# Optimization experiments

Measured on AMD Instinct MI355X. Metric: run time of the kernel, lower is better.

## Reference

```python
import jax, jax.numpy as jnp
import numpy as np

BITS = 4
PACK = 32 // BITS            # 8 nibbles per int32
IN, OUT = 4096, 4096
NNZ = 75008


def setup_inputs() -> dict:
    key = jax.random.key(0)
    ks = jax.random.split(key, 7)
    x = jax.random.normal(ks[0], (4, 2048, IN), jnp.float32)
    # packed 4-bit indices: any int32 bit pattern is valid after masking
    qweight = jax.random.randint(ks[1], (IN // PACK, OUT), 0, 2147483647, jnp.int32)
    lookup_table = jax.random.normal(ks[2], (OUT, 2 ** BITS), jnp.float32)
    bias = jax.random.normal(ks[3], (OUT,), jnp.float32)
    rows = jnp.sort(jax.random.randint(ks[4], (OUT + 1,), 0, NNZ, jnp.int32))
    outlier_rows = rows.at[0].set(0).at[-1].set(NNZ)  # valid CSR crow
    outlier_cols = jax.random.randint(ks[5], (NNZ,), 0, IN, jnp.int32)
    outlier_vals = jax.random.normal(ks[6], (NNZ,), jnp.float32)
    return {
        'x': x,
        'lookup_table': lookup_table,
        'bias': bias,
        'outlier_vals': outlier_vals,
        'qweight': qweight,
        'outlier_rows': outlier_rows,
        'outlier_cols': outlier_cols,
    }


def _dequant_weight(qweight, lookup_table):
    # unpack 8 4-bit indices per int32 along the packed-infeatures axis
    shifts = (jnp.arange(PACK, dtype=jnp.int32) * BITS)
    idx = ((qweight[:, None, :] >> shifts[None, :, None]) & 0xF)  # [IN//8, 8, OUT]
    idx = idx.reshape(IN, OUT)                                     # [IN, OUT]
    # per-output-channel LUT gather: W[o, i] = lut[o, idx[i, o]]
    return jnp.take_along_axis(lookup_table, idx.T, axis=1)       # [OUT, IN]


def reference(x, lookup_table, bias, outlier_vals, qweight, outlier_rows, outlier_cols):
    W = _dequant_weight(qweight, lookup_table)
    # CSR outlier correction: scatter-add sparse values into the dense weight
    row_ids = jnp.clip(
        jnp.searchsorted(outlier_rows, jnp.arange(NNZ, dtype=jnp.int32), side='right') - 1,
        0, OUT - 1)
    W = W.at[row_ids, outlier_cols].add(outlier_vals)
    x2 = x.reshape(-1, IN)
    y = x2 @ W.T + bias                                            # [B, OUT]
    return y.reshape(x.shape[:-1] + (OUT,))
```

## Files before the change

### kernel.cpp

```cpp
#include <hip/hip_runtime.h>
#include <stdint.h>

#define IN_F  4096
#define OUT_F 4096

typedef unsigned short u16;
typedef __attribute__((ext_vector_type(8))) short bf16x8;
typedef __attribute__((ext_vector_type(4))) float f32x4;

__device__ __forceinline__ u16 f2bf(float f) {
    union { float f; unsigned u; } c; c.f = f;
    unsigned u = c.u;
    return (u16)((u + 0x7FFFu + ((u >> 16) & 1u)) >> 16);
}
__device__ __forceinline__ float bf2f(u16 h) {
    union { unsigned u; float f; } c; c.u = ((unsigned)h) << 16;
    return c.f;
}

__device__ __forceinline__ void load_lds16(const void* g, void* l) {
    unsigned loff = (unsigned)(uintptr_t)l;
    loff = (unsigned)__builtin_amdgcn_readfirstlane((int)loff);
    __builtin_amdgcn_global_load_lds(
        (const __attribute__((address_space(1))) void*)(uintptr_t)g,
        (__attribute__((address_space(3))) void*)(uintptr_t)loff,
        16, 0, 0);
}

#define DQ_O 64
#define DQ_I 256
#define DQ_BLOCKS ((IN_F / DQ_I) * (OUT_F / DQ_O))

__global__ __launch_bounds__(256) void prep_k(const int* __restrict__ qw,
                                              const float* __restrict__ lut,
                                              const int* __restrict__ rows,
                                              const int* __restrict__ cols,
                                              const float* __restrict__ vals,
                                              u16* __restrict__ W,
                                              const float4* __restrict__ x,
                                              u16* __restrict__ xb) {
    __shared__ __align__(16) u16 sW[DQ_O * DQ_I];
    __shared__ u16 slut[DQ_O * 18];

    const int tid = threadIdx.x;

    if (blockIdx.x >= DQ_BLOCKS) {
        const size_t i = (size_t)(blockIdx.x - DQ_BLOCKS) * 256 + tid;
        const float4 a = x[2 * i];
        const float4 b = x[2 * i + 1];
        union { u16 h[8]; uint4 v; } u;
        u.h[0] = f2bf(a.x); u.h[1] = f2bf(a.y); u.h[2] = f2bf(a.z); u.h[3] = f2bf(a.w);
        u.h[4] = f2bf(b.x); u.h[5] = f2bf(b.y); u.h[6] = f2bf(b.z); u.h[7] = f2bf(b.w);
        *(uint4*)(xb + i * 8) = u.v;
        return;
    }

    const int o0 = (blockIdx.x >> 4) * DQ_O;
    const int i0 = (blockIdx.x & 15) * DQ_I;
    const int p0 = i0 >> 3;

    {
        const int idx = tid * 4;
        const float4 v = *(const float4*)(lut + (size_t)o0 * 16 + idx);
        u16* d = slut + (idx >> 4) * 18 + (idx & 15);
        d[0] = f2bf(v.x); d[1] = f2bf(v.y); d[2] = f2bf(v.z); d[3] = f2bf(v.w);
    }
    __syncthreads();

    const int o_l = tid & 63;
    const int swz = o_l & 31;
#pragma unroll
    for (int it = 0; it < 8; ++it) {
        const int p = (tid >> 6) + it * 4;
        const unsigned w = (unsigned)qw[(size_t)(p0 + p) * OUT_F + (o0 + o_l)];
        union { u16 h[8]; uint4 v; } u;
#pragma unroll
        for (int j = 0; j < 8; ++j)
            u.h[j] = slut[o_l * 18 + ((w >> (4 * j)) & 15u)];
        *(uint4*)(sW + o_l * DQ_I + ((p ^ swz) << 3)) = u.v;
    }
    __syncthreads();

    if (tid < DQ_O) {
        const int s = rows[o0 + tid], e = rows[o0 + tid + 1];
        int k = s;
#define APPLY(CJ, VV) do {                                                  \
        const unsigned j_ = (unsigned)((CJ) - i0);                          \
        if (j_ < DQ_I) {                                                    \
            u16* p16 = sW + tid * DQ_I + (((j_ >> 3) ^ swz) << 3) + (j_ & 7); \
            *p16 = f2bf(bf2f(*p16) + (VV));                                 \
        } } while (0)
        for (; k + 4 <= e; k += 4) {
            const int c0 = cols[k], c1 = cols[k + 1], c2 = cols[k + 2], c3 = cols[k + 3];
            const float v0 = vals[k], v1 = vals[k + 1], v2 = vals[k + 2], v3 = vals[k + 3];
            APPLY(c0, v0); APPLY(c1, v1); APPLY(c2, v2); APPLY(c3, v3);
        }
        for (; k < e; ++k) APPLY(cols[k], vals[k]);
#undef APPLY
    }
    __syncthreads();

    const int ch = tid & 31;
#pragma unroll
    for (int it = 0; it < 8; ++it) {
        const int r = (tid >> 5) + it * 8;
        *(uint4*)(W + (size_t)(o0 + r) * IN_F + i0 + ch * 8) =
            *(const uint4*)(sW + r * DQ_I + ((ch ^ (r & 31)) << 3));
    }
}

#define GK 4096

#define MF(A_, B_, C_) __builtin_amdgcn_mfma_f32_16x16x32_bf16(A_, B_, C_, 0, 0, 0)

#define STAGE_A(SLOT, KC) do {                                              \
    load_lds16(srcA0 + (KC) * 64, ldsA + (SLOT) * 16384 + ldst);            \
    load_lds16(srcA1 + (KC) * 64, ldsA + (SLOT) * 16384 + 8192 + ldst);     \
  } while (0)
#define STAGE_B(SLOT, KC) do {                                              \
    load_lds16(srcB0 + (KC) * 64, ldsB + (SLOT) * 16384 + ldst);            \
    load_lds16(srcB1 + (KC) * 64, ldsB + (SLOT) * 16384 + 8192 + ldst);     \
  } while (0)

#define WAIT4 asm volatile("s_waitcnt vmcnt(4)" ::: "memory")
#define VNOP  ((void)0)

#define LDA(S, M) (*(const bf16x8*)(ldsA + (S) * 16384 + (M) * 1024 + aoff))
#define LDB(S, N) (*(const bf16x8*)(ldsB + (S) * 16384 + (N) * 1024 + boff))

#define RD_ALO(S) aA0 = LDA(S, 0); aA1 = LDA(S, 1); aA2 = LDA(S, 2); aA3 = LDA(S, 3)
#define RD_AHI(S) aB0 = LDA(S, 4); aB1 = LDA(S, 5); aB2 = LDA(S, 6); aB3 = LDA(S, 7)
#define RD_BA(S)  bA0 = LDB(S, 0); bA1 = LDB(S, 1); bA2 = LDB(S, 2); bA3 = LDB(S, 3)
#define RD_BB(S)  bB0 = LDB(S, 0); bB1 = LDB(S, 1); bB2 = LDB(S, 2); bB3 = LDB(S, 3)

#define MFMA16(A0, A1, A2, A3, B0, B1, B2, B3, R)                           \
    acc[(R)+0][0] = MF(A0, B0, acc[(R)+0][0]);                              \
    acc[(R)+0][1] = MF(A0, B1, acc[(R)+0][1]);                              \
    acc[(R)+0][2] = MF(A0, B2, acc[(R)+0][2]);                              \
    acc[(R)+0][3] = MF(A0, B3, acc[(R)+0][3]);                              \
    acc[(R)+1][0] = MF(A1, B0, acc[(R)+1][0]);                              \
    acc[(R)+1][1] = MF(A1, B1, acc[(R)+1][1]);                              \
    acc[(R)+1][2] = MF(A1, B2, acc[(R)+1][2]);                              \
    acc[(R)+1][3] = MF(A1, B3, acc[(R)+1][3]);                              \
    acc[(R)+2][0] = MF(A2, B0, acc[(R)+2][0]);                              \
    acc[(R)+2][1] = MF(A2, B1, acc[(R)+2][1]);                              \
    acc[(R)+2][2] = MF(A2, B2, acc[(R)+2][2]);                              \
    acc[(R)+2][3] = MF(A2, B3, acc[(R)+2][3]);                              \
    acc[(R)+3][0] = MF(A3, B0, acc[(R)+3][0]);                              \
    acc[(R)+3][1] = MF(A3, B1, acc[(R)+3][1]);                              \
    acc[(R)+3][2] = MF(A3, B2, acc[(R)+3][2]);                              \
    acc[(R)+3][3] = MF(A3, B3, acc[(R)+3][3]);

#define PHASE(RDNEXT, STG, A0, A1, A2, A3, B0, B1, B2, B3, R, VM)           \
  { RDNEXT;                                                                 \
    STG;                                                                    \
    __builtin_amdgcn_s_setprio(1);                                          \
    MFMA16(A0, A1, A2, A3, B0, B1, B2, B3, R)                               \
    __builtin_amdgcn_s_setprio(0);                                          \
    VM;                                                                     \
    __builtin_amdgcn_s_barrier(); }

__global__ __launch_bounds__(512, 2) void gemm8_k(const u16* __restrict__ A,
                                                  const u16* __restrict__ B,
                                                  const float* __restrict__ bias,
                                                  float* __restrict__ C,
                                                  int M, int N) {
    __shared__ __align__(16) u16 sAq[4 * 256 * 32];
    __shared__ __align__(16) u16 sBq[4 * 256 * 32];

    const int tid  = threadIdx.x;
    const int wave = tid >> 6;
    const int lane = tid & 63;

    const int ntx = N >> 8;
    const int nwg = (M >> 8) * ntx;
    const int cpx = nwg >> 3;
    const int bid = blockIdx.x;
    const int wg  = (bid & 7) * cpx + (bid >> 3);
    const int bm = (wg / ntx) << 8;
    const int bn = (wg % ntx) << 8;

    const int r4  = tid >> 2;
    const int cbs = ((tid & 3) << 4) ^ (((r4 >> 1) & 3) << 4);
    const char* srcA0 = (const char*)A + ((size_t)(bm + r4) * GK) * 2 + cbs;
    const char* srcA1 = (const char*)A + ((size_t)(bm + 128 + r4) * GK) * 2 + cbs;
    const char* srcB0 = (const char*)B + ((size_t)(bn + r4) * GK) * 2 + cbs;
    const char* srcB1 = (const char*)B + ((size_t)(bn + 128 + r4) * GK) * 2 + cbs;

    char* ldsA = (char*)sAq;
    char* ldsB = (char*)sBq;
    const int ldst = wave << 10;

    const int frow = lane & 15;
    const int fk2  = (lane >> 4) << 4;
    const int fswz = ((frow >> 1) & 3) << 4;
    const int wmr  = (wave >> 2) << 7;
    const int wnr  = (wave & 3) << 6;
    const int aoff = ((wmr + frow) << 6) + (fk2 ^ fswz);
    const int boff = ((wnr + frow) << 6) + (fk2 ^ fswz);

    f32x4 acc[8][4] = {};
    bf16x8 aA0, aA1, aA2, aA3, aB0, aB1, aB2, aB3;
    bf16x8 bA0, bA1, bA2, bA3, bB0, bB1, bB2, bB3;

    STAGE_A(0, 0); STAGE_B(0, 0);
    STAGE_A(1, 1); STAGE_B(1, 1);
    STAGE_A(2, 2); STAGE_B(2, 2);
    WAIT4;
    __builtin_amdgcn_s_barrier();
    RD_ALO(0); RD_BA(0);

    for (int it = 0; it < 32; ++it) {
        const int c   = it * 4;
        const int kc3 = c + 3;
        const int kc4 = (c + 4) & 127;
        const int kc5 = (c + 5) & 127;
        const int kc6 = (c + 6) & 127;

        PHASE(RD_AHI(0),            STAGE_A(3, kc3), aA0, aA1, aA2, aA3, bA0, bA1, bA2, bA3, 0, VNOP)
        PHASE(RD_ALO(1); RD_BB(1),  STAGE_B(3, kc3), aB0, aB1, aB2, aB3, bA0, bA1, bA2, bA3, 4, WAIT4)
        PHASE(RD_AHI(1),            STAGE_A(0, kc4), aA0, aA1, aA2, aA3, bB0, bB1, bB2, bB3, 0, VNOP)
        PHASE(RD_ALO(2); RD_BA(2),  STAGE_B(0, kc4), aB0, aB1, aB2, aB3, bB0, bB1, bB2, bB3, 4, WAIT4)
        PHASE(RD_AHI(2),            STAGE_A(1, kc5), aA0, aA1, aA2, aA3, bA0, bA1, bA2, bA3, 0, VNOP)
        PHASE(RD_ALO(3); RD_BB(3),  STAGE_B(1, kc5), aB0, aB1, aB2, aB3, bA0, bA1, bA2, bA3, 4, WAIT4)
        PHASE(RD_AHI(3),            STAGE_A(2, kc6), aA0, aA1, aA2, aA3, bB0, bB1, bB2, bB3, 0, VNOP)
        PHASE(RD_ALO(0); RD_BA(0),  STAGE_B(2, kc6), aB0, aB1, aB2, aB3, bB0, bB1, bB2, bB3, 4, WAIT4)
    }

    const int cm = bm + wmr;
    const int cn = bn + wnr;
#pragma unroll
    for (int n = 0; n < 4; ++n) {
        const int col = cn + n * 16 + frow;
        const float bv = bias[col];
#pragma unroll
        for (int m = 0; m < 8; ++m) {
            const int r0 = cm + m * 16 + (lane >> 4) * 4;
#pragma unroll
            for (int r = 0; r < 4; ++r)
                C[(size_t)(r0 + r) * N + col] = acc[m][n][r] + bv;
        }
    }
}

extern "C" void kernel_launch(void* const* d_in, const int* in_sizes, int n_in,
                              void* d_out, int out_size, void* d_ws, size_t ws_size,
                              hipStream_t stream) {
    (void)n_in; (void)out_size; (void)ws_size;
    const float* x     = (const float*)d_in[0];
    const float* lut   = (const float*)d_in[1];
    const float* bias  = (const float*)d_in[2];
    const float* ovals = (const float*)d_in[3];
    const int*   qw    = (const int*)d_in[4];
    const int*   orows = (const int*)d_in[5];
    const int*   ocols = (const int*)d_in[6];
    float* y = (float*)d_out;

    const int M = in_sizes[0] / IN_F;

    u16* W  = (u16*)d_ws;
    u16* xb = (u16*)((char*)d_ws + (size_t)OUT_F * IN_F * 2);

    const int cvt_blocks = (int)((size_t)M * IN_F / 8 / 256);
    prep_k<<<DQ_BLOCKS + cvt_blocks, 256, 0, stream>>>(
        qw, lut, orows, ocols, ovals, W, (const float4*)x, xb);

    const int nwg = (M / 256) * (OUT_F / 256);
    gemm8_k<<<dim3(nwg), dim3(512), 0, stream>>>(xb, W, bias, y, M, OUT_F);
}
```

Measured before the change: 471.6 us.

## Switch GEMM inner loop from 16x16x32 to 32x32x16 bf16 MFMA tiles

```diff
diff --git a/kernel.cpp b/kernel.cpp
--- a/kernel.cpp
+++ b/kernel.cpp
@@ -6,7 +6,7 @@
 
 typedef unsigned short u16;
 typedef __attribute__((ext_vector_type(8))) short bf16x8;
-typedef __attribute__((ext_vector_type(4))) float f32x4;
+typedef __attribute__((ext_vector_type(16))) float f32x16;
 
 __device__ __forceinline__ u16 f2bf(float f) {
     union { float f; unsigned u; } c; c.f = f;
@@ -111,7 +111,7 @@
 
 #define GK 4096
 
-#define MF(A_, B_, C_) __builtin_amdgcn_mfma_f32_16x16x32_bf16(A_, B_, C_, 0, 0, 0)
+#define MF32(A_, B_, C_) __builtin_amdgcn_mfma_f32_32x32x16_bf16(A_, B_, C_, 0, 0, 0)
 
 #define STAGE_A(SLOT, KC) do {                                              \
     load_lds16(srcA0 + (KC) * 64, ldsA + (SLOT) * 16384 + ldst);            \
@@ -125,37 +125,29 @@
 #define WAIT4 asm volatile("s_waitcnt vmcnt(4)" ::: "memory")
 #define VNOP  ((void)0)
 
-#define LDA(S, M) (*(const bf16x8*)(ldsA + (S) * 16384 + (M) * 1024 + aoff))
-#define LDB(S, N) (*(const bf16x8*)(ldsB + (S) * 16384 + (N) * 1024 + boff))
-
-#define RD_ALO(S) aA0 = LDA(S, 0); aA1 = LDA(S, 1); aA2 = LDA(S, 2); aA3 = LDA(S, 3)
-#define RD_AHI(S) aB0 = LDA(S, 4); aB1 = LDA(S, 5); aB2 = LDA(S, 6); aB3 = LDA(S, 7)
-#define RD_BA(S)  bA0 = LDB(S, 0); bA1 = LDB(S, 1); bA2 = LDB(S, 2); bA3 = LDB(S, 3)
-#define RD_BB(S)  bB0 = LDB(S, 0); bB1 = LDB(S, 1); bB2 = LDB(S, 2); bB3 = LDB(S, 3)
-
-#define MFMA16(A0, A1, A2, A3, B0, B1, B2, B3, R)                           \
-    acc[(R)+0][0] = MF(A0, B0, acc[(R)+0][0]);                              \
-    acc[(R)+0][1] = MF(A0, B1, acc[(R)+0][1]);                              \
-    acc[(R)+0][2] = MF(A0, B2, acc[(R)+0][2]);                              \
-    acc[(R)+0][3] = MF(A0, B3, acc[(R)+0][3]);                              \
-    acc[(R)+1][0] = MF(A1, B0, acc[(R)+1][0]);                              \
-    acc[(R)+1][1] = MF(A1, B1, acc[(R)+1][1]);                              \
-    acc[(R)+1][2] = MF(A1, B2, acc[(R)+1][2]);                              \
-    acc[(R)+1][3] = MF(A1, B3, acc[(R)+1][3]);                              \
-    acc[(R)+2][0] = MF(A2, B0, acc[(R)+2][0]);                              \
-    acc[(R)+2][1] = MF(A2, B1, acc[(R)+2][1]);                              \
-    acc[(R)+2][2] = MF(A2, B2, acc[(R)+2][2]);                              \
-    acc[(R)+2][3] = MF(A2, B3, acc[(R)+2][3]);                              \
-    acc[(R)+3][0] = MF(A3, B0, acc[(R)+3][0]);                              \
-    acc[(R)+3][1] = MF(A3, B1, acc[(R)+3][1]);                              \
-    acc[(R)+3][2] = MF(A3, B2, acc[(R)+3][2]);                              \
-    acc[(R)+3][3] = MF(A3, B3, acc[(R)+3][3]);
-
-#define PHASE(RDNEXT, STG, A0, A1, A2, A3, B0, B1, B2, B3, R, VM)           \
+#define LDA32(S, M, AO) (*(const bf16x8*)(ldsA + (S) * 16384 + (M) * 2048 + (AO)))
+#define LDB32(S, N, BO) (*(const bf16x8*)(ldsB + (S) * 16384 + (N) * 2048 + (BO)))
+
+#define RD_SETA(S, AO, BO)                                                  \
+    aA0 = LDA32(S, 0, AO); aA1 = LDA32(S, 1, AO);                           \
+    aA2 = LDA32(S, 2, AO); aA3 = LDA32(S, 3, AO);                           \
+    bA0 = LDB32(S, 0, BO); bA1 = LDB32(S, 1, BO)
+#define RD_SETB(S, AO, BO)                                                  \
+    aB0 = LDA32(S, 0, AO); aB1 = LDA32(S, 1, AO);                           \
+    aB2 = LDA32(S, 2, AO); aB3 = LDA32(S, 3, AO);                           \
+    bB0 = LDB32(S, 0, BO); bB1 = LDB32(S, 1, BO)
+
+#define MFMA8(A0, A1, A2, A3, B0, B1)                                       \
+    acc00 = MF32(A0, B0, acc00); acc01 = MF32(A0, B1, acc01);               \
+    acc10 = MF32(A1, B0, acc10); acc11 = MF32(A1, B1, acc11);               \
+    acc20 = MF32(A2, B0, acc20); acc21 = MF32(A2, B1, acc21);               \
+    acc30 = MF32(A3, B0, acc30); acc31 = MF32(A3, B1, acc31);
+
+#define PHASE(RDNEXT, STG, MFMAS, VM)                                       \
   { RDNEXT;                                                                 \
     STG;                                                                    \
     __builtin_amdgcn_s_setprio(1);                                          \
-    MFMA16(A0, A1, A2, A3, B0, B1, B2, B3, R)                               \
+    MFMAS;                                                                  \
     __builtin_amdgcn_s_setprio(0);                                          \
     VM;                                                                     \
     __builtin_amdgcn_s_barrier(); }
@@ -191,24 +183,27 @@
     char* ldsB = (char*)sBq;
     const int ldst = wave << 10;
 
-    const int frow = lane & 15;
-    const int fk2  = (lane >> 4) << 4;
-    const int fswz = ((frow >> 1) & 3) << 4;
+    const int l31  = lane & 31;
+    const int fswz = ((l31 >> 1) & 3) << 4;
+    const int kb   = (lane >> 5) << 4;
     const int wmr  = (wave >> 2) << 7;
     const int wnr  = (wave & 3) << 6;
-    const int aoff = ((wmr + frow) << 6) + (fk2 ^ fswz);
-    const int boff = ((wnr + frow) << 6) + (fk2 ^ fswz);
-
-    f32x4 acc[8][4] = {};
-    bf16x8 aA0, aA1, aA2, aA3, aB0, aB1, aB2, aB3;
-    bf16x8 bA0, bA1, bA2, bA3, bB0, bB1, bB2, bB3;
+    const int aoff0 = ((wmr + l31) << 6) + (kb ^ fswz);
+    const int aoff1 = ((wmr + l31) << 6) + ((32 | kb) ^ fswz);
+    const int boff0 = ((wnr + l31) << 6) + (kb ^ fswz);
+    const int boff1 = ((wnr + l31) << 6) + ((32 | kb) ^ fswz);
+
+    f32x16 acc00 = {}, acc01 = {}, acc10 = {}, acc11 = {};
+    f32x16 acc20 = {}, acc21 = {}, acc30 = {}, acc31 = {};
+    bf16x8 aA0, aA1, aA2, aA3, bA0, bA1;
+    bf16x8 aB0, aB1, aB2, aB3, bB0, bB1;
 
     STAGE_A(0, 0); STAGE_B(0, 0);
     STAGE_A(1, 1); STAGE_B(1, 1);
     STAGE_A(2, 2); STAGE_B(2, 2);
     WAIT4;
     __builtin_amdgcn_s_barrier();
-    RD_ALO(0); RD_BA(0);
+    RD_SETA(0, aoff0, boff0);
 
     for (int it = 0; it < 32; ++it) {
         const int c   = it * 4;
@@ -217,30 +212,39 @@
         const int kc5 = (c + 5) & 127;
         const int kc6 = (c + 6) & 127;
 
-        PHASE(RD_AHI(0),            STAGE_A(3, kc3), aA0, aA1, aA2, aA3, bA0, bA1, bA2, bA3, 0, VNOP)
-        PHASE(RD_ALO(1); RD_BB(1),  STAGE_B(3, kc3), aB0, aB1, aB2, aB3, bA0, bA1, bA2, bA3, 4, WAIT4)
-        PHASE(RD_AHI(1),            STAGE_A(0, kc4), aA0, aA1, aA2, aA3, bB0, bB1, bB2, bB3, 0, VNOP)
-        PHASE(RD_ALO(2); RD_BA(2),  STAGE_B(0, kc4), aB0, aB1, aB2, aB3, bB0, bB1, bB2, bB3, 4, WAIT4)
-        PHASE(RD_AHI(2),            STAGE_A(1, kc5), aA0, aA1, aA2, aA3, bA0, bA1, bA2, bA3, 0, VNOP)
-        PHASE(RD_ALO(3); RD_BB(3),  STAGE_B(1, kc5), aB0, aB1, aB2, aB3, bA0, bA1, bA2, bA3, 4, WAIT4)
-        PHASE(RD_AHI(3),            STAGE_A(2, kc6), aA0, aA1, aA2, aA3, bB0, bB1, bB2, bB3, 0, VNOP)
-        PHASE(RD_ALO(0); RD_BA(0),  STAGE_B(2, kc6), aB0, aB1, aB2, aB3, bB0, bB1, bB2, bB3, 4, WAIT4)
-    }
-
-    const int cm = bm + wmr;
+        PHASE(RD_SETB(0, aoff1, boff1), STAGE_A(3, kc3),
+              MFMA8(aA0, aA1, aA2, aA3, bA0, bA1), VNOP)
+        PHASE(RD_SETA(1, aoff0, boff0), STAGE_B(3, kc3),
+              MFMA8(aB0, aB1, aB2, aB3, bB0, bB1), WAIT4)
+        PHASE(RD_SETB(1, aoff1, boff1), STAGE_A(0, kc4),
+              MFMA8(aA0, aA1, aA2, aA3, bA0, bA1), VNOP)
+        PHASE(RD_SETA(2, aoff0, boff0), STAGE_B(0, kc4),
+              MFMA8(aB0, aB1, aB2, aB3, bB0, bB1), WAIT4)
+        PHASE(RD_SETB(2, aoff1, boff1), STAGE_A(1, kc5),
+              MFMA8(aA0, aA1, aA2, aA3, bA0, bA1), VNOP)
+        PHASE(RD_SETA(3, aoff0, boff0), STAGE_B(1, kc5),
+              MFMA8(aB0, aB1, aB2, aB3, bB0, bB1), WAIT4)
+        PHASE(RD_SETB(3, aoff1, boff1), STAGE_A(2, kc6),
+              MFMA8(aA0, aA1, aA2, aA3, bA0, bA1), VNOP)
+        PHASE(RD_SETA(0, aoff0, boff0), STAGE_B(2, kc6),
+              MFMA8(aB0, aB1, aB2, aB3, bB0, bB1), WAIT4)
+    }
+
+    const int cm = bm + wmr + ((lane >> 5) << 2);
     const int cn = bn + wnr;
-#pragma unroll
-    for (int n = 0; n < 4; ++n) {
-        const int col = cn + n * 16 + frow;
-        const float bv = bias[col];
-#pragma unroll
-        for (int m = 0; m < 8; ++m) {
-            const int r0 = cm + m * 16 + (lane >> 4) * 4;
-#pragma unroll
-            for (int r = 0; r < 4; ++r)
-                C[(size_t)(r0 + r) * N + col] = acc[m][n][r] + bv;
-        }
-    }
+#define EPI(ACC, FM, FN) do {                                               \
+        const int col = cn + (FN) * 32 + l31;                               \
+        const float bv = bias[col];                                         \
+        const int rb = cm + (FM) * 32;                                      \
+        _Pragma("unroll")                                                   \
+        for (int r = 0; r < 16; ++r)                                        \
+            C[(size_t)(rb + (r & 3) + 8 * (r >> 2)) * N + col] = ACC[r] + bv; \
+    } while (0)
+    EPI(acc00, 0, 0); EPI(acc01, 0, 1);
+    EPI(acc10, 1, 0); EPI(acc11, 1, 1);
+    EPI(acc20, 2, 0); EPI(acc21, 2, 1);
+    EPI(acc30, 3, 0); EPI(acc31, 3, 1);
+#undef EPI
 }
 
 extern "C" void kernel_launch(void* const* d_in, const int* in_sizes, int n_in,
```

Result: slower. 484.5 us (+2.7%).
